# Kernel tuning notes

Measured on AMD Instinct MI355X. Metric: run time of the kernel, lower is better.

Reference implementation:

```python
import jax, jax.numpy as jnp
import numpy as np

N, E = 100000, 1600000
IN_F, HID, OUT_F, HEADS = 256, 128, 64, 1
C = HID // HEADS  # per-head channels (=128 for heads=1)
NEG_SLOPE = 0.2   # PyG GATConv default leaky_relu slope


def setup_inputs() -> dict:
    key = jax.random.key(0)
    ks = jax.random.split(key, 16)
    w = lambda k, shape, fan: (jax.random.normal(k, shape, jnp.float32) / np.float32(np.sqrt(fan)))
    return {
        "x": jax.random.normal(ks[0], (N, IN_F), jnp.float32),
        "edge_index": jax.random.randint(ks[1], (2, E), 0, N, dtype=jnp.int32),
        "W_in": w(ks[2], (IN_F, HID), IN_F),
        "b_in": jnp.zeros((HID,), jnp.float32),
        "W1": w(ks[3], (HID, HEADS * C), HID),
        "att_src1": w(ks[4], (HEADS, C), C),
        "att_dst1": w(ks[5], (HEADS, C), C),
        "bias1": jnp.zeros((C,), jnp.float32),
        "W2": w(ks[6], (HID, HEADS * C), HID),
        "att_src2": w(ks[7], (HEADS, C), C),
        "att_dst2": w(ks[8], (HEADS, C), C),
        "bias2": jnp.zeros((C,), jnp.float32),
        "W_out": w(ks[9], (HID, OUT_F), HID),
        "b_out": jnp.zeros((OUT_F,), jnp.float32),
    }


def gat_conv(h, src, dst, W, a_src, a_dst, bias):
    """PyG GATConv, concat=False: per-head attention, segment softmax over dst, mean over heads."""
    g = (h @ W).reshape(-1, HEADS, C)                      # [N,H,C]
    alpha_src = jnp.einsum("nhc,hc->nh", g, a_src)         # [N,H]
    alpha_dst = jnp.einsum("nhc,hc->nh", g, a_dst)         # [N,H]
    e = jax.nn.leaky_relu(alpha_src[src] + alpha_dst[dst], NEG_SLOPE)  # [E,H]
    m = jax.ops.segment_max(e, dst, num_segments=N)        # [N,H], -inf for empty segments
    m = jnp.where(jnp.isfinite(m), m, 0.0)
    p = jnp.exp(e - m[dst])
    s = jax.ops.segment_sum(p, dst, num_segments=N)        # [N,H]
    alpha = p / (s[dst] + 1e-16)                           # [E,H]
    msg = g[src] * alpha[..., None]                        # [E,H,C]  (dominant traffic)
    out = jax.ops.segment_sum(msg, dst, num_segments=N)    # [N,H,C]
    return out.mean(axis=1) + bias                         # concat=False -> head average


def reference(x, edge_index, W_in, b_in, W1, att_src1, att_dst1, bias1,
              W2, att_src2, att_dst2, bias2, W_out, b_out):
    src, dst = edge_index[0], edge_index[1]
    h = x @ W_in + b_in
    h = jax.nn.relu(gat_conv(h, src, dst, W1, att_src1, att_dst1, bias1))
    h = jax.nn.relu(gat_conv(h, src, dst, W2, att_src2, att_dst2, bias2))
    return h @ W_out + b_out
```

## Files before the change

### kernel.cpp

```cpp
#include <hip/hip_runtime.h>
#include <hip/hip_fp16.h>
#include <math.h>

#define NN 100000
#define EE 1600000
constexpr int IN_F = 256, HID = 128, OUT_F = 64;

#define NB 196
#define CAP 16384
#define CH 4096
#define NCHUNK 391

typedef __bf16    bf16x8 __attribute__((ext_vector_type(8)));
typedef _Float16  h16x8  __attribute__((ext_vector_type(8)));
typedef float     f32x4  __attribute__((ext_vector_type(4)));

__device__ __forceinline__ f32x4 mfma16b(bf16x8 a, bf16x8 b, f32x4 c){
  return __builtin_amdgcn_mfma_f32_16x16x32_bf16(a, b, c, 0, 0, 0);
}
__device__ __forceinline__ f32x4 mfma16h(h16x8 a, h16x8 b, f32x4 c){
  return __builtin_amdgcn_mfma_f32_16x16x32_f16(a, b, c, 0, 0, 0);
}

__device__ __forceinline__ void fmamix2(float& aLo, float& aHi, __half2 g2, float al){
  asm("v_fma_mix_f32 %0, %2, %3, %0 op_sel:[0,0,0] op_sel_hi:[1,0,0]\n\t"
      "v_fma_mix_f32 %1, %2, %3, %1 op_sel:[1,0,0] op_sel_hi:[1,0,0]"
      : "+v"(aLo), "+v"(aHi) : "v"(g2), "v"(al));
}

__device__ __forceinline__ float wred_max(float v){
#pragma unroll
  for (int m=1; m<64; m<<=1) v = fmaxf(v, __shfl_xor(v, m, 64));
  return v;
}
__device__ __forceinline__ float wred_sum(float v){
#pragma unroll
  for (int m=1; m<64; m<<=1) v += __shfl_xor(v, m, 64);
  return v;
}

__device__ __forceinline__ unsigned fkey(float x){
  unsigned u = __float_as_uint(x);
  return (u & 0x80000000u) ? ~u : (u ^ 0x80000000u);
}
__device__ __forceinline__ float funkey(unsigned k){
  return __uint_as_float((k & 0x80000000u) ? (k ^ 0x80000000u) : ~k);
}

__global__ __launch_bounds__(256) void k_bin(const int* __restrict__ src,
    const int* __restrict__ dst, int* __restrict__ bucketCnt, int* __restrict__ recs)
{
  __shared__ int cnt[NB];
  __shared__ int base[NB];
  const int tid = threadIdx.x;
  const int e0 = blockIdx.x * CH;
  const int ne = min(CH, EE - e0);

  for (int i=tid; i<NB; i+=256) cnt[i] = 0;
  __syncthreads();
  for (int i=tid; i<ne; i+=256) atomicAdd(&cnt[dst[e0+i]>>9], 1);
  __syncthreads();
  for (int i=tid; i<NB; i+=256) base[i] = atomicAdd(&bucketCnt[i], cnt[i]);
  __syncthreads();
  for (int i=tid; i<NB; i+=256) cnt[i] = 0;
  __syncthreads();
  for (int i=tid; i<ne; i+=256){
    int d = dst[e0+i], b = d >> 9;
    int r = atomicAdd(&cnt[b], 1);
    int pos = base[b] + r;
    if (pos < CAP) recs[(size_t)b*CAP + pos] = src[e0+i] | ((d & 511) << 17);
  }
}

__global__ void k_bscan(const int* __restrict__ bucketCnt, int* __restrict__ bucketStart){
  __shared__ int sd[256];
  int t = threadIdx.x;
  int v = (t < NB) ? min(bucketCnt[t], CAP) : 0;
  sd[t] = v; __syncthreads();
#pragma unroll
  for (int off=1; off<256; off<<=1){
    int x = (t >= off) ? sd[t-off] : 0;
    __syncthreads();
    sd[t] += x;
    __syncthreads();
  }
  if (t < NB) bucketStart[t] = sd[t] - v;
}

__global__ __launch_bounds__(512) void k_csr(const int* __restrict__ recs,
    const int* __restrict__ bucketCnt, const int* __restrict__ bucketStart,
    int* __restrict__ rp, int* __restrict__ colsrc)
{
  __shared__ int hist[513];
  __shared__ int srcbuf[CAP];
  const int tid = threadIdx.x;
  const int b = blockIdx.x;
  const int cntb = min(bucketCnt[b], CAP);
  const int bstart = bucketStart[b];
  const int n0 = b << 9;
  const int nnode = min(512, NN - n0);
  const int* rb = recs + (size_t)b*CAP;

  if (tid < 513) hist[tid] = 0;
  if (tid == 511) hist[512] = 0;
  __syncthreads();
  for (int i=tid; i<cntb; i+=512) atomicAdd(&hist[(rb[i] >> 17) + 1], 1);
  __syncthreads();
#pragma unroll
  for (int off=1; off<513; off<<=1){
    int v0 = (tid >= off) ? hist[tid-off] : 0;
    int i1 = tid + 512;
    int v1 = (i1 < 513 && i1 >= off) ? hist[i1-off] : 0;
    __syncthreads();
    hist[tid] += v0;
    if (i1 < 513) hist[i1] += v1;
    __syncthreads();
  }
  for (int l=tid; l<nnode; l+=512) rp[n0+l] = bstart + hist[l];
  if (b == 0 && tid == 0) rp[NN] = EE;
  __syncthreads();
  for (int i=tid; i<cntb; i+=512){
    int rec = rb[i];
    int r = atomicAdd(&hist[rec >> 17], 1);
    srcbuf[r] = rec & 0x1FFFF;
  }
  __syncthreads();
  for (int i=tid; i<cntb; i+=512) colsrc[bstart + i] = srcbuf[i];
}

__global__ void k_wsplit(const float* __restrict__ W, __bf16* __restrict__ hi, __bf16* __restrict__ lo,
                         int K, int N){
  int idx = blockIdx.x*256 + threadIdx.x;
  if (idx >= K*N) return;
  int k = idx / N, n = idx - k*N;
  float v = W[idx];
  __bf16 h = (__bf16)v;
  hi[(size_t)n*K + k] = h;
  lo[(size_t)n*K + k] = (__bf16)(v - (float)h);
}
__global__ void k_wsplit16(const float* __restrict__ W, _Float16* __restrict__ hi, _Float16* __restrict__ lo,
                           int K, int N){
  int idx = blockIdx.x*256 + threadIdx.x;
  if (idx >= K*N) return;
  int k = idx / N, n = idx - k*N;
  float v = W[idx] * 16.f;
  _Float16 h = (_Float16)v;
  hi[(size_t)n*K + k] = h;
  lo[(size_t)n*K + k] = (_Float16)(v - (float)h);
}

__global__ __launch_bounds__(256, 2) void k_gemm_in(
    const float* __restrict__ A, const __bf16* __restrict__ Bhi, const __bf16* __restrict__ Blo,
    const float* __restrict__ bias, __half* __restrict__ C, int nrows)
{
  constexpr int K = 256, BN = 128, NF = 8;
  __shared__ __bf16 Ah[256][36];
  __shared__ __bf16 Al[256][36];
  __shared__ __bf16 Bh[BN][36];
  __shared__ __bf16 Bl[BN][36];
  const int tid = threadIdx.x, w = tid >> 6, lane = tid & 63;
  const int lr = lane & 15, lk = (lane >> 4) * 8;
  const int rowBase = blockIdx.x * 256;

  f32x4 acc[4][NF];
#pragma unroll
  for (int f=0; f<4; f++)
#pragma unroll
    for (int nf=0; nf<NF; nf++) acc[f][nf] = (f32x4)(0.f);

  const int bn = tid >> 1, bo = (tid & 1) * 16;

  for (int kc=0; kc<K; kc+=32){
    float4 av[8];
#pragma unroll
    for (int k8=0; k8<8; k8++){
      int P = tid + 256*k8;
      int r = P >> 3, pc = P & 7;
      int gr = rowBase + r; if (gr >= nrows) gr = nrows - 1;
      av[k8] = *(const float4*)(A + (size_t)gr*K + kc + pc*4);
    }
    bf16x8 bh0, bh1, bl0, bl1;
    {
      const __bf16* ph = Bhi + (size_t)bn*K + kc + bo;
      const __bf16* pl = Blo + (size_t)bn*K + kc + bo;
      bh0 = *(const bf16x8*)(ph);  bh1 = *(const bf16x8*)(ph + 8);
      bl0 = *(const bf16x8*)(pl);  bl1 = *(const bf16x8*)(pl + 8);
    }
    __syncthreads();
#pragma unroll
    for (int k8=0; k8<8; k8++){
      int P = tid + 256*k8;
      int r = P >> 3, pc = P & 7;
      float fv[4] = {av[k8].x, av[k8].y, av[k8].z, av[k8].w};
      __bf16 h4[4], l4[4];
#pragma unroll
      for (int u=0; u<4; u++){
        __bf16 h = (__bf16)fv[u];
        h4[u] = h; l4[u] = (__bf16)(fv[u] - (float)h);
      }
      *(uint2*)&Ah[r][pc*4] = *(uint2*)h4;
      *(uint2*)&Al[r][pc*4] = *(uint2*)l4;
    }
    *(bf16x8*)&Bh[bn][bo]     = bh0;  *(bf16x8*)&Bh[bn][bo + 8] = bh1;
    *(bf16x8*)&Bl[bn][bo]     = bl0;  *(bf16x8*)&Bl[bn][bo + 8] = bl1;
    __syncthreads();

    bf16x8 fah[4], fal[4];
#pragma unroll
    for (int f=0; f<4; f++){
      fah[f] = *(const bf16x8*)&Ah[w*64 + f*16 + lr][lk];
      fal[f] = *(const bf16x8*)&Al[w*64 + f*16 + lr][lk];
    }
#pragma unroll
    for (int nf=0; nf<NF; nf++){
      bf16x8 bh = *(const bf16x8*)&Bh[nf*16 + lr][lk];
#pragma unroll
      for (int f=0; f<4; f++) acc[f][nf] = mfma16b(fah[f], bh, acc[f][nf]);
#pragma unroll
      for (int f=0; f<4; f++) acc[f][nf] = mfma16b(fal[f], bh, acc[f][nf]);
      bf16x8 bl = *(const bf16x8*)&Bl[nf*16 + lr][lk];
#pragma unroll
      for (int f=0; f<4; f++) acc[f][nf] = mfma16b(fah[f], bl, acc[f][nf]);
    }
  }

  const int rq = lane >> 4;
#pragma unroll
  for (int f=0; f<4; f++){
    const int rbase = rowBase + w*64 + f*16 + rq*4;
#pragma unroll
    for (int i=0; i<4; i++){
      int row = rbase + i;
      if (row < nrows){
#pragma unroll
        for (int nf=0; nf<NF; nf++){
          float v = acc[f][nf][i] + bias[nf*16 + lr];
          C[(size_t)row*BN + nf*16 + lr] = __float2half(v);
        }
      }
    }
  }
}

template<int K, int BN, bool ATT, bool BIAS, int OMODE>
__global__ __launch_bounds__(256, 2) void k_gemm_f16(
    const _Float16* __restrict__ A, const _Float16* __restrict__ Whi,
    const _Float16* __restrict__ Wlo, const float* __restrict__ bias,
    void* __restrict__ C0, const float* __restrict__ attS, const float* __restrict__ attD,
    float* __restrict__ asrc, float* __restrict__ adst,
    unsigned* __restrict__ gk, int nrows)
{
  constexpr int NF = BN/16;
  __shared__ _Float16 Ah[256][72];
  __shared__ _Float16 Bh[BN][72];
  __shared__ _Float16 Bl[BN][72];
  const int tid = threadIdx.x, w = tid >> 6, lane = tid & 63;
  const int lr = lane & 15, lk = (lane >> 4) * 8;
  const int rowBase = blockIdx.x * 256;

  f32x4 acc[4][NF];
#pragma unroll
  for (int f=0; f<4; f++)
#pragma unroll
    for (int nf=0; nf<NF; nf++) acc[f][nf] = (f32x4)(0.f);

  const bool bact = tid < BN*2;
  const int bn = tid >> 1, bo = (tid & 1) * 32;

  for (int kc=0; kc<K; kc+=64){
    h16x8 av[8];
#pragma unroll
    for (int k8=0; k8<8; k8++){
      int P = tid + 256*k8;
      int r = P >> 3, pc = P & 7;
      int gr = rowBase + r; if (gr >= nrows) gr = nrows - 1;
      av[k8] = *(const h16x8*)(A + (size_t)gr*K + kc + pc*8);
    }
    h16x8 bhv[4], blv[4];
    if (bact){
#pragma unroll
      for (int q=0; q<4; q++){
        bhv[q] = *(const h16x8*)(Whi + (size_t)bn*K + kc + bo + q*8);
        blv[q] = *(const h16x8*)(Wlo + (size_t)bn*K + kc + bo + q*8);
      }
    }
    __syncthreads();
#pragma unroll
    for (int k8=0; k8<8; k8++){
      int P = tid + 256*k8;
      int r = P >> 3, pc = P & 7;
      *(h16x8*)&Ah[r][pc*8] = av[k8];
    }
    if (bact){
#pragma unroll
      for (int q=0; q<4; q++){
        *(h16x8*)&Bh[bn][bo + q*8] = bhv[q];
        *(h16x8*)&Bl[bn][bo + q*8] = blv[q];
      }
    }
    __syncthreads();

#pragma unroll
    for (int ks=0; ks<64; ks+=32){
      h16x8 fah[4];
#pragma unroll
      for (int f=0; f<4; f++) fah[f] = *(const h16x8*)&Ah[w*64 + f*16 + lr][ks + lk];
#pragma unroll
      for (int nf=0; nf<NF; nf++){
        h16x8 bh = *(const h16x8*)&Bh[nf*16 + lr][ks + lk];
#pragma unroll
        for (int f=0; f<4; f++) acc[f][nf] = mfma16h(fah[f], bh, acc[f][nf]);
        h16x8 bl = *(const h16x8*)&Bl[nf*16 + lr][ks + lk];
#pragma unroll
        for (int f=0; f<4; f++) acc[f][nf] = mfma16h(fah[f], bl, acc[f][nf]);
      }
    }
  }
#pragma unroll
  for (int f=0; f<4; f++)
#pragma unroll
    for (int nf=0; nf<NF; nf++) acc[f][nf] *= 0.0625f;

  const int rq = lane >> 4;
  float pmax = -3e38f;
#pragma unroll
  for (int f=0; f<4; f++){
    const int rbase = rowBase + w*64 + f*16 + rq*4;
    if (ATT){
      float ps[4] = {0.f,0.f,0.f,0.f}, pd[4] = {0.f,0.f,0.f,0.f};
#pragma unroll
      for (int nf=0; nf<NF; nf++){
        float sv = attS[nf*16 + lr], dv = attD[nf*16 + lr];
#pragma unroll
        for (int i=0;i<4;i++){
          ps[i] = fmaf(acc[f][nf][i], sv, ps[i]);
          pd[i] = fmaf(acc[f][nf][i], dv, pd[i]);
        }
      }
#pragma unroll
      for (int mm=1; mm<16; mm<<=1){
#pragma unroll
        for (int i=0;i<4;i++){
          ps[i] += __shfl_xor(ps[i], mm, 64);
          pd[i] += __shfl_xor(pd[i], mm, 64);
        }
      }
      if (lr == 0){
#pragma unroll
        for (int i=0;i<4;i++){
          int row = rbase + i;
          if (row < nrows){ asrc[row] = ps[i]; adst[row] = pd[i]; }
        }
        pmax = fmaxf(pmax, fmaxf(fmaxf(ps[0],ps[1]), fmaxf(ps[2],ps[3])));
      }
    }
#pragma unroll
    for (int i=0;i<4;i++){
      int row = rbase + i;
      if (row < nrows){
#pragma unroll
        for (int nf=0; nf<NF; nf++){
          float v = acc[f][nf][i] + (BIAS ? bias[nf*16 + lr] : 0.f);
          size_t cidx = (size_t)row*BN + nf*16 + lr;
          if constexpr (OMODE == 0) ((float*)C0)[cidx] = v;
          else                      ((__half*)C0)[cidx] = __float2half(v);
        }
      }
    }
  }
  if (ATT){
    pmax = wred_max(pmax);
    if (lane == 0) atomicMax(gk, fkey(pmax));
  }
}

__global__ __launch_bounds__(512) void k_alpha(
    const float* __restrict__ asrc, const float* __restrict__ adst,
    const int* __restrict__ rp, const int* __restrict__ cs,
    const unsigned* __restrict__ gkey, int2* __restrict__ epack)
{
  int w = threadIdx.x >> 6, lane = threadIdx.x & 63;
  int node = blockIdx.x*8 + w;
  if (node >= NN) return;
  int r0 = rp[node], deg = rp[node+1] - r0;
  if (deg == 0) return;
  float ad = adst[node];
  float tC = funkey(*gkey) + ad;
  float C = (tC > 0.f) ? tC : 0.2f*tC;

  float p0 = 0.f, p1 = 0.f; int s0 = 0, s1 = 0;
  float ssum = 0.f;
  for (int i = lane; i < deg; i += 64){
    int s = cs[r0 + i];
    float t = asrc[s] + ad;
    float e = (t > 0.f) ? t : 0.2f*t;
    float p = __expf(e - C);
    ssum += p;
    if (i < 64)       { p0 = p; s0 = s; }
    else if (i < 128) { p1 = p; s1 = s; }
  }
  ssum = wred_sum(ssum);
  float inv = 1.f/(ssum + 1e-16f);
  if (lane < deg)      epack[r0 + lane]      = make_int2(s0, __float_as_int(p0*inv));
  if (64 + lane < deg) epack[r0 + 64 + lane] = make_int2(s1, __float_as_int(p1*inv));
  for (int i = 128 + lane; i < deg; i += 64){
    int s = cs[r0 + i];
    float t = asrc[s] + ad;
    float e = (t > 0.f) ? t : 0.2f*t;
    epack[r0 + i] = make_int2(s, __float_as_int(__expf(e - C)*inv));
  }
}

__global__ __launch_bounds__(512) void k_gather(const __half* __restrict__ g,
    const int2* __restrict__ epack, const int* __restrict__ rp,
    const float* __restrict__ bias, __half* __restrict__ out)
{
  int w = threadIdx.x >> 6, lane = threadIdx.x & 63;
  int node = blockIdx.x*8 + w;
  if (node >= NN) return;
  int r0 = rp[node], deg = rp[node+1] - r0;
  const int eg = lane >> 4, cl = lane & 15;
  const __half* gcl = g + cl*8;

  float a[8] = {0.f,0.f,0.f,0.f,0.f,0.f,0.f,0.f};
  int nst = (deg + 3) >> 2;

  int2 eA = make_int2(0,0), eB = make_int2(0,0);
  float4 gA = make_float4(0,0,0,0), gB = make_float4(0,0,0,0);
  if (nst > 0){
    if (eg < deg) eA = epack[r0 + eg];
    gA = *(const float4*)(gcl + (size_t)eA.x * HID);
  }
  if (nst > 1){
    int i1 = 4 + eg;
    if (i1 < deg) eB = epack[r0 + i1];
    gB = *(const float4*)(gcl + (size_t)eB.x * HID);
  }
  for (int j = 0; j < nst; j += 2){
    {
      float al = __int_as_float(eA.y); float4 cur = gA;
      if (j + 2 < nst){
        int ii = 4*(j+2) + eg;
        eA = (ii < deg) ? epack[r0 + ii] : make_int2(0,0);
        gA = *(const float4*)(gcl + (size_t)eA.x * HID);
      }
      const __half2* hp = (const __half2*)&cur;
      fmamix2(a[0], a[1], hp[0], al);
      fmamix2(a[2], a[3], hp[1], al);
      fmamix2(a[4], a[5], hp[2], al);
      fmamix2(a[6], a[7], hp[3], al);
    }
    if (j + 1 < nst){
      float al = __int_as_float(eB.y); float4 cur = gB;
      if (j + 3 < nst){
        int ii = 4*(j+3) + eg;
        eB = (ii < deg) ? epack[r0 + ii] : make_int2(0,0);
        gB = *(const float4*)(gcl + (size_t)eB.x * HID);
      }
      const __half2* hp = (const __half2*)&cur;
      fmamix2(a[0], a[1], hp[0], al);
      fmamix2(a[2], a[3], hp[1], al);
      fmamix2(a[4], a[5], hp[2], al);
      fmamix2(a[6], a[7], hp[3], al);
    }
  }
#pragma unroll
  for (int u=0; u<8; u++){
    a[u] += __shfl_xor(a[u], 16, 64);
    a[u] += __shfl_xor(a[u], 32, 64);
  }
  if (eg == 0){
    __half hv[8];
#pragma unroll
    for (int u=0; u<8; u++)
      hv[u] = __float2half(fmaxf(a[u] + bias[cl*8 + u], 0.f));
    *(float4*)(out + (size_t)node*HID + cl*8) = *(float4*)hv;
  }
}

extern "C" void kernel_launch(void* const* d_in, const int* in_sizes, int n_in,
                              void* d_out, int out_size, void* d_ws, size_t ws_size,
                              hipStream_t stream) {
  const float* x     = (const float*)d_in[0];
  const int*   ei    = (const int*)  d_in[1];
  const float* W_in  = (const float*)d_in[2];
  const float* b_in  = (const float*)d_in[3];
  const float* W1    = (const float*)d_in[4];
  const float* as1   = (const float*)d_in[5];
  const float* ad1   = (const float*)d_in[6];
  const float* bias1 = (const float*)d_in[7];
  const float* W2    = (const float*)d_in[8];
  const float* as2   = (const float*)d_in[9];
  const float* ad2   = (const float*)d_in[10];
  const float* bias2 = (const float*)d_in[11];
  const float* W_out = (const float*)d_in[12];
  const float* b_out = (const float*)d_in[13];
  float* out = (float*)d_out;

  char* ws = (char*)d_ws;
  size_t off = 0;
  auto alloc = [&](size_t bytes)->void*{ void* p = ws + off; off += (bytes + 255) & ~255ull; return p; };
  __half*   H    = (__half*)  alloc((size_t)NN*HID*2);
  __half*   G    = (__half*)  alloc((size_t)NN*HID*2);
  __half*   O1   = (__half*)  alloc((size_t)NN*HID*2);
  float*    asrc = (float*)   alloc((size_t)NN*4);
  float*    adst = (float*)   alloc((size_t)NN*4);
  int*      rp   = (int*)     alloc((size_t)(NN+1)*4);
  int*      colsrc = (int*)   alloc((size_t)EE*4);
  int2*     epack  = (int2*)  alloc((size_t)EE*8);
  int*      recs   = (int*)   alloc((size_t)NB*CAP*4);
  int*      bucketCnt   = (int*)alloc(NB*4);
  int*      bucketStart = (int*)alloc(NB*4);
  unsigned* gk1 = (unsigned*)alloc(4);
  unsigned* gk2 = (unsigned*)alloc(4);
  __bf16*   whiI = (__bf16*) alloc((size_t)HID*IN_F*2);
  __bf16*   wloI = (__bf16*) alloc((size_t)HID*IN_F*2);
  _Float16* w1h  = (_Float16*)alloc((size_t)HID*HID*2);
  _Float16* w1l  = (_Float16*)alloc((size_t)HID*HID*2);
  _Float16* w2h  = (_Float16*)alloc((size_t)HID*HID*2);
  _Float16* w2l  = (_Float16*)alloc((size_t)HID*HID*2);
  _Float16* wOh  = (_Float16*)alloc((size_t)OUT_F*HID*2);
  _Float16* wOl  = (_Float16*)alloc((size_t)OUT_F*HID*2);
  (void)ws_size; (void)in_sizes; (void)n_in; (void)out_size;

  const int* srcIdx = ei;
  const int* dstIdx = ei + EE;

  k_wsplit  <<<(IN_F*HID+255)/256, 256, 0, stream>>>(W_in,  whiI, wloI, IN_F, HID);
  k_wsplit16<<<(HID*HID+255)/256, 256, 0, stream>>>(W1,    w1h, w1l, HID, HID);
  k_wsplit16<<<(HID*HID+255)/256, 256, 0, stream>>>(W2,    w2h, w2l, HID, HID);
  k_wsplit16<<<(HID*OUT_F+255)/256, 256, 0, stream>>>(W_out, wOh, wOl, HID, OUT_F);

  hipMemsetAsync(bucketCnt, 0, NB*4, stream);
  hipMemsetAsync(gk1, 0, 4, stream);
  hipMemsetAsync(gk2, 0, 4, stream);
  k_bin  <<<NCHUNK, 256, 0, stream>>>(srcIdx, dstIdx, bucketCnt, recs);
  k_bscan<<<1, 256, 0, stream>>>(bucketCnt, bucketStart);
  k_csr  <<<NB, 512, 0, stream>>>(recs, bucketCnt, bucketStart, rp, colsrc);

  const int gblocks = (NN + 255) / 256;
  const int ablocks = (NN + 7) / 8;
  k_gemm_in<<<gblocks, 256, 0, stream>>>(x, whiI, wloI, b_in, H, NN);
  k_gemm_f16<128,128,true,false,1><<<gblocks, 256, 0, stream>>>(
      (const _Float16*)H, w1h, w1l, nullptr, G, as1, ad1, asrc, adst, gk1, NN);
  k_alpha <<<ablocks, 512, 0, stream>>>(asrc, adst, rp, colsrc, gk1, epack);
  k_gather<<<ablocks, 512, 0, stream>>>(G, epack, rp, bias1, O1);
  k_gemm_f16<128,128,true,false,1><<<gblocks, 256, 0, stream>>>(
      (const _Float16*)O1, w2h, w2l, nullptr, G, as2, ad2, asrc, adst, gk2, NN);
  k_alpha <<<ablocks, 512, 0, stream>>>(asrc, adst, rp, colsrc, gk2, epack);
  k_gather<<<ablocks, 512, 0, stream>>>(G, epack, rp, bias2, (__half*)H);
  k_gemm_f16<128,64,false,true,0><<<gblocks, 256, 0, stream>>>(
      (const _Float16*)H, wOh, wOl, b_out, out, nullptr, nullptr, nullptr, nullptr, nullptr, NN);
}
```

Before: 349.9 us.

## Merge weight-split kernels and memsets, shrink GEMM LDS tiles, deepen gather prefetch

Folds the four weight-split launches into one kernel and the three memsets into one, which trims launch overhead. In the GEMM kernels it raises the occupancy hint from 2 to 3 blocks, cuts LDS padding, and moves the f16 GEMM to a 32-wide K step, so each block uses less shared memory. The gather kernel goes from a 2-deep to a 4-deep software prefetch of edge records and feature rows, keeping more loads in flight. The risks are higher register pressure from the deeper prefetch and more LDS bank conflicts from the smaller padding.

```diff
diff --git a/kernel.cpp b/kernel.cpp
--- a/kernel.cpp
+++ b/kernel.cpp
@@ -128,36 +128,49 @@
   for (int i=tid; i<cntb; i+=512) colsrc[bstart + i] = srcbuf[i];
 }
 
-__global__ void k_wsplit(const float* __restrict__ W, __bf16* __restrict__ hi, __bf16* __restrict__ lo,
-                         int K, int N){
+__global__ void k_wsplit_all(
+    const float* __restrict__ W_in, __bf16* __restrict__ whiI, __bf16* __restrict__ wloI,
+    const float* __restrict__ W1, _Float16* __restrict__ w1h, _Float16* __restrict__ w1l,
+    const float* __restrict__ W2, _Float16* __restrict__ w2h, _Float16* __restrict__ w2l,
+    const float* __restrict__ W_out, _Float16* __restrict__ wOh, _Float16* __restrict__ wOl)
+{
   int idx = blockIdx.x*256 + threadIdx.x;
-  if (idx >= K*N) return;
-  int k = idx / N, n = idx - k*N;
-  float v = W[idx];
-  __bf16 h = (__bf16)v;
-  hi[(size_t)n*K + k] = h;
-  lo[(size_t)n*K + k] = (__bf16)(v - (float)h);
-}
-__global__ void k_wsplit16(const float* __restrict__ W, _Float16* __restrict__ hi, _Float16* __restrict__ lo,
-                           int K, int N){
-  int idx = blockIdx.x*256 + threadIdx.x;
-  if (idx >= K*N) return;
-  int k = idx / N, n = idx - k*N;
-  float v = W[idx] * 16.f;
-  _Float16 h = (_Float16)v;
-  hi[(size_t)n*K + k] = h;
-  lo[(size_t)n*K + k] = (_Float16)(v - (float)h);
-}
-
-__global__ __launch_bounds__(256, 2) void k_gemm_in(
+  if (idx < 32768){
+    int k = idx >> 7, n = idx & 127;
+    float v = W_in[idx];
+    __bf16 h = (__bf16)v;
+    whiI[n*256 + k] = h;
+    wloI[n*256 + k] = (__bf16)(v - (float)h);
+  } else if (idx < 49152){
+    int i = idx - 32768, k = i >> 7, n = i & 127;
+    float v = W1[i] * 16.f;
+    _Float16 h = (_Float16)v;
+    w1h[n*128 + k] = h;
+    w1l[n*128 + k] = (_Float16)(v - (float)h);
+  } else if (idx < 65536){
+    int i = idx - 49152, k = i >> 7, n = i & 127;
+    float v = W2[i] * 16.f;
+    _Float16 h = (_Float16)v;
+    w2h[n*128 + k] = h;
+    w2l[n*128 + k] = (_Float16)(v - (float)h);
+  } else if (idx < 73728){
+    int i = idx - 65536, k = i / 64, n = i - k*64;
+    float v = W_out[i] * 16.f;
+    _Float16 h = (_Float16)v;
+    wOh[n*128 + k] = h;
+    wOl[n*128 + k] = (_Float16)(v - (float)h);
+  }
+}
+
+__global__ __launch_bounds__(256, 3) void k_gemm_in(
     const float* __restrict__ A, const __bf16* __restrict__ Bhi, const __bf16* __restrict__ Blo,
     const float* __restrict__ bias, __half* __restrict__ C, int nrows)
 {
   constexpr int K = 256, BN = 128, NF = 8;
-  __shared__ __bf16 Ah[256][36];
-  __shared__ __bf16 Al[256][36];
-  __shared__ __bf16 Bh[BN][36];
-  __shared__ __bf16 Bl[BN][36];
+  __shared__ __bf16 Ah[256][34];
+  __shared__ __bf16 Al[256][34];
+  __shared__ __bf16 Bh[BN][34];
+  __shared__ __bf16 Bl[BN][34];
   const int tid = threadIdx.x, w = tid >> 6, lane = tid & 63;
   const int lr = lane & 15, lk = (lane >> 4) * 8;
   const int rowBase = blockIdx.x * 256;
@@ -243,7 +256,7 @@
 }
 
 template<int K, int BN, bool ATT, bool BIAS, int OMODE>
-__global__ __launch_bounds__(256, 2) void k_gemm_f16(
+__global__ __launch_bounds__(256, 3) void k_gemm_f16(
     const _Float16* __restrict__ A, const _Float16* __restrict__ Whi,
     const _Float16* __restrict__ Wlo, const float* __restrict__ bias,
     void* __restrict__ C0, const float* __restrict__ attS, const float* __restrict__ attD,
@@ -251,9 +264,9 @@
     unsigned* __restrict__ gk, int nrows)
 {
   constexpr int NF = BN/16;
-  __shared__ _Float16 Ah[256][72];
-  __shared__ _Float16 Bh[BN][72];
-  __shared__ _Float16 Bl[BN][72];
+  __shared__ _Float16 Ah[256][40];
+  __shared__ _Float16 Bh[BN][40];
+  __shared__ _Float16 Bl[BN][40];
   const int tid = threadIdx.x, w = tid >> 6, lane = tid & 63;
   const int lr = lane & 15, lk = (lane >> 4) * 8;
   const int rowBase = blockIdx.x * 256;
@@ -265,55 +278,48 @@
     for (int nf=0; nf<NF; nf++) acc[f][nf] = (f32x4)(0.f);
 
   const bool bact = tid < BN*2;
-  const int bn = tid >> 1, bo = (tid & 1) * 32;
-
-  for (int kc=0; kc<K; kc+=64){
-    h16x8 av[8];
-#pragma unroll
-    for (int k8=0; k8<8; k8++){
-      int P = tid + 256*k8;
-      int r = P >> 3, pc = P & 7;
+  const int bn = tid >> 1, bo = (tid & 1) * 16;
+
+  for (int kc=0; kc<K; kc+=32){
+    h16x8 av[4];
+#pragma unroll
+    for (int k4=0; k4<4; k4++){
+      int P = tid + 256*k4;
+      int r = P >> 2, pc = P & 3;
       int gr = rowBase + r; if (gr >= nrows) gr = nrows - 1;
-      av[k8] = *(const h16x8*)(A + (size_t)gr*K + kc + pc*8);
-    }
-    h16x8 bhv[4], blv[4];
+      av[k4] = *(const h16x8*)(A + (size_t)gr*K + kc + pc*8);
+    }
+    h16x8 bh0, bh1, bl0, bl1;
     if (bact){
-#pragma unroll
-      for (int q=0; q<4; q++){
-        bhv[q] = *(const h16x8*)(Whi + (size_t)bn*K + kc + bo + q*8);
-        blv[q] = *(const h16x8*)(Wlo + (size_t)bn*K + kc + bo + q*8);
-      }
-    }
-    __syncthreads();
-#pragma unroll
-    for (int k8=0; k8<8; k8++){
-      int P = tid + 256*k8;
-      int r = P >> 3, pc = P & 7;
-      *(h16x8*)&Ah[r][pc*8] = av[k8];
+      const _Float16* ph = Whi + (size_t)bn*K + kc + bo;
+      const _Float16* pl = Wlo + (size_t)bn*K + kc + bo;
+      bh0 = *(const h16x8*)(ph);  bh1 = *(const h16x8*)(ph + 8);
+      bl0 = *(const h16x8*)(pl);  bl1 = *(const h16x8*)(pl + 8);
+    }
+    __syncthreads();
+#pragma unroll
+    for (int k4=0; k4<4; k4++){
+      int P = tid + 256*k4;
+      int r = P >> 2, pc = P & 3;
+      *(h16x8*)&Ah[r][pc*8] = av[k4];
     }
     if (bact){
-#pragma unroll
-      for (int q=0; q<4; q++){
-        *(h16x8*)&Bh[bn][bo + q*8] = bhv[q];
-        *(h16x8*)&Bl[bn][bo + q*8] = blv[q];
-      }
-    }
-    __syncthreads();
-
-#pragma unroll
-    for (int ks=0; ks<64; ks+=32){
-      h16x8 fah[4];
-#pragma unroll
-      for (int f=0; f<4; f++) fah[f] = *(const h16x8*)&Ah[w*64 + f*16 + lr][ks + lk];
-#pragma unroll
-      for (int nf=0; nf<NF; nf++){
-        h16x8 bh = *(const h16x8*)&Bh[nf*16 + lr][ks + lk];
-#pragma unroll
-        for (int f=0; f<4; f++) acc[f][nf] = mfma16h(fah[f], bh, acc[f][nf]);
-        h16x8 bl = *(const h16x8*)&Bl[nf*16 + lr][ks + lk];
-#pragma unroll
-        for (int f=0; f<4; f++) acc[f][nf] = mfma16h(fah[f], bl, acc[f][nf]);
-      }
+      *(h16x8*)&Bh[bn][bo]     = bh0;  *(h16x8*)&Bh[bn][bo + 8] = bh1;
+      *(h16x8*)&Bl[bn][bo]     = bl0;  *(h16x8*)&Bl[bn][bo + 8] = bl1;
+    }
+    __syncthreads();
+
+    h16x8 fah[4];
+#pragma unroll
+    for (int f=0; f<4; f++) fah[f] = *(const h16x8*)&Ah[w*64 + f*16 + lr][lk];
+#pragma unroll
+    for (int nf=0; nf<NF; nf++){
+      h16x8 bh = *(const h16x8*)&Bh[nf*16 + lr][lk];
+#pragma unroll
+      for (int f=0; f<4; f++) acc[f][nf] = mfma16h(fah[f], bh, acc[f][nf]);
+      h16x8 bl = *(const h16x8*)&Bl[nf*16 + lr][lk];
+#pragma unroll
+      for (int f=0; f<4; f++) acc[f][nf] = mfma16h(fah[f], bl, acc[f][nf]);
     }
   }
 #pragma unroll
@@ -421,49 +427,45 @@
   int r0 = rp[node], deg = rp[node+1] - r0;
   const int eg = lane >> 4, cl = lane & 15;
   const __half* gcl = g + cl*8;
+  const int2* ep = epack + r0 + eg;
 
   float a[8] = {0.f,0.f,0.f,0.f,0.f,0.f,0.f,0.f};
   int nst = (deg + 3) >> 2;
 
-  int2 eA = make_int2(0,0), eB = make_int2(0,0);
-  float4 gA = make_float4(0,0,0,0), gB = make_float4(0,0,0,0);
-  if (nst > 0){
-    if (eg < deg) eA = epack[r0 + eg];
-    gA = *(const float4*)(gcl + (size_t)eA.x * HID);
-  }
-  if (nst > 1){
-    int i1 = 4 + eg;
-    if (i1 < deg) eB = epack[r0 + i1];
-    gB = *(const float4*)(gcl + (size_t)eB.x * HID);
-  }
-  for (int j = 0; j < nst; j += 2){
-    {
-      float al = __int_as_float(eA.y); float4 cur = gA;
-      if (j + 2 < nst){
-        int ii = 4*(j+2) + eg;
-        eA = (ii < deg) ? epack[r0 + ii] : make_int2(0,0);
-        gA = *(const float4*)(gcl + (size_t)eA.x * HID);
-      }
-      const __half2* hp = (const __half2*)&cur;
-      fmamix2(a[0], a[1], hp[0], al);
-      fmamix2(a[2], a[3], hp[1], al);
-      fmamix2(a[4], a[5], hp[2], al);
-      fmamix2(a[6], a[7], hp[3], al);
-    }
-    if (j + 1 < nst){
-      float al = __int_as_float(eB.y); float4 cur = gB;
-      if (j + 3 < nst){
-        int ii = 4*(j+3) + eg;
-        eB = (ii < deg) ? epack[r0 + ii] : make_int2(0,0);
-        gB = *(const float4*)(gcl + (size_t)eB.x * HID);
-      }
-      const __half2* hp = (const __half2*)&cur;
-      fmamix2(a[0], a[1], hp[0], al);
-      fmamix2(a[2], a[3], hp[1], al);
-      fmamix2(a[4], a[5], hp[2], al);
-      fmamix2(a[6], a[7], hp[3], al);
-    }
-  }
+  int2 e0 = make_int2(0,0), e1 = e0, e2 = e0, e3 = e0;
+  if (0 < nst && eg < deg)        e0 = ep[0];
+  if (1 < nst && 4  + eg < deg)   e1 = ep[4];
+  if (2 < nst && 8  + eg < deg)   e2 = ep[8];
+  if (3 < nst && 12 + eg < deg)   e3 = ep[12];
+  float4 g0 = *(const float4*)(gcl + ((size_t)((unsigned)e0.x << 7)));
+  float4 g1 = *(const float4*)(gcl + ((size_t)((unsigned)e1.x << 7)));
+  float4 g2 = *(const float4*)(gcl + ((size_t)((unsigned)e2.x << 7)));
+  float4 g3 = *(const float4*)(gcl + ((size_t)((unsigned)e3.x << 7)));
+
+#define GSTEP(EV, GV, SOFF)                                                  \
+  {                                                                          \
+    float al = __int_as_float(EV.y); float4 cur = GV;                        \
+    int nj = j + 4 + SOFF;                                                   \
+    if (nj < nst){                                                           \
+      int idx = 4*nj + eg;                                                   \
+      EV = (idx < deg) ? ep[4*nj] : make_int2(0,0);                          \
+      GV = *(const float4*)(gcl + ((size_t)((unsigned)EV.x << 7)));          \
+    }                                                                        \
+    const __half2* hp = (const __half2*)&cur;                                \
+    fmamix2(a[0], a[1], hp[0], al);                                          \
+    fmamix2(a[2], a[3], hp[1], al);                                          \
+    fmamix2(a[4], a[5], hp[2], al);                                          \
+    fmamix2(a[6], a[7], hp[3], al);                                          \
+  }
+
+  for (int j = 0; j < nst; j += 4){
+    GSTEP(e0, g0, 0)
+    if (j + 1 < nst) GSTEP(e1, g1, 1)
+    if (j + 2 < nst) GSTEP(e2, g2, 2)
+    if (j + 3 < nst) GSTEP(e3, g3, 3)
+  }
+#undef GSTEP
+
 #pragma unroll
   for (int u=0; u<8; u++){
     a[u] += __shfl_xor(a[u], 16, 64);
@@ -509,10 +511,11 @@
   int*      colsrc = (int*)   alloc((size_t)EE*4);
   int2*     epack  = (int2*)  alloc((size_t)EE*8);
   int*      recs   = (int*)   alloc((size_t)NB*CAP*4);
-  int*      bucketCnt   = (int*)alloc(NB*4);
+  int*      misc   = (int*)   alloc((size_t)(NB+2)*4);
+  int*      bucketCnt = misc;
+  unsigned* gk1 = (unsigned*)(misc + NB);
+  unsigned* gk2 = (unsigned*)(misc + NB + 1);
   int*      bucketStart = (int*)alloc(NB*4);
-  unsigned* gk1 = (unsigned*)alloc(4);
-  unsigned* gk2 = (unsigned*)alloc(4);
   __bf16*   whiI = (__bf16*) alloc((size_t)HID*IN_F*2);
   __bf16*   wloI = (__bf16*) alloc((size_t)HID*IN_F*2);
   _Float16* w1h  = (_Float16*)alloc((size_t)HID*HID*2);
@@ -526,14 +529,9 @@
   const int* srcIdx = ei;
   const int* dstIdx = ei + EE;
 
-  k_wsplit  <<<(IN_F*HID+255)/256, 256, 0, stream>>>(W_in,  whiI, wloI, IN_F, HID);
-  k_wsplit16<<<(HID*HID+255)/256, 256, 0, stream>>>(W1,    w1h, w1l, HID, HID);
-  k_wsplit16<<<(HID*HID+255)/256, 256, 0, stream>>>(W2,    w2h, w2l, HID, HID);
-  k_wsplit16<<<(HID*OUT_F+255)/256, 256, 0, stream>>>(W_out, wOh, wOl, HID, OUT_F);
-
-  hipMemsetAsync(bucketCnt, 0, NB*4, stream);
-  hipMemsetAsync(gk1, 0, 4, stream);
-  hipMemsetAsync(gk2, 0, 4, stream);
+  k_wsplit_all<<<288, 256, 0, stream>>>(W_in, whiI, wloI, W1, w1h, w1l, W2, w2h, w2l, W_out, wOh, wOl);
+  hipMemsetAsync(misc, 0, (size_t)(NB+2)*4, stream);
+
   k_bin  <<<NCHUNK, 256, 0, stream>>>(srcIdx, dstIdx, bucketCnt, recs);
   k_bscan<<<1, 256, 0, stream>>>(bucketCnt, bucketStart);
   k_csr  <<<NB, 512, 0, stream>>>(recs, bucketCnt, bucketStart, rp, colsrc);
```

After: 496.9 us. 42.0% more time.
